# Optimization experiments

Measured on AMD Instinct MI355X. Metric: run time of the kernel, lower is better.

Reference implementation:

```python
import jax, jax.numpy as jnp
import numpy as np

NUM_CLASSES = 2
THRESH = 0.5        # overlap_thresh
NEGPOS = 3          # neg:pos ratio
VAR = (0.1, 0.2)    # cfg['variance']
B, P, O = 64, 32768, 50


def point_form(p):
    # center-size [cx,cy,w,h] -> corner [xmin,ymin,xmax,ymax]
    return jnp.concatenate([p[:, :2] - p[:, 2:] * 0.5, p[:, :2] + p[:, 2:] * 0.5], axis=1)


def iou(a, b):
    # a [O,4], b [P,4] corner form -> [O,P]
    lt = jnp.maximum(a[:, None, :2], b[None, :, :2])
    rb = jnp.minimum(a[:, None, 2:], b[None, :, 2:])
    wh = jnp.clip(rb - lt, 0.0, None)
    inter = wh[..., 0] * wh[..., 1]
    area_a = ((a[:, 2] - a[:, 0]) * (a[:, 3] - a[:, 1]))[:, None]
    area_b = ((b[:, 2] - b[:, 0]) * (b[:, 3] - b[:, 1]))[None, :]
    return inter / (area_a + area_b - inter)


def encode(matched, priors_cs):
    g_cxcy = ((matched[:, :2] + matched[:, 2:]) * 0.5 - priors_cs[:, :2]) / (VAR[0] * priors_cs[:, 2:])
    g_wh = jnp.log((matched[:, 2:] - matched[:, :2]) / priors_cs[:, 2:]) / VAR[1]
    return jnp.concatenate([g_cxcy, g_wh], axis=1)


def match_one(truths, labels, priors_cs, priors_pt):
    ovl = iou(truths, priors_pt)                # [O,P]
    best_prior_idx = jnp.argmax(ovl, axis=1)    # [O] best prior per GT
    best_truth_ovl = jnp.max(ovl, axis=0)       # [P]
    best_truth_idx = jnp.argmax(ovl, axis=0)    # [P]
    best_truth_ovl = best_truth_ovl.at[best_prior_idx].set(2.0)
    best_truth_idx = best_truth_idx.at[best_prior_idx].set(jnp.arange(truths.shape[0]))
    matched = truths[best_truth_idx]            # [P,4]
    conf = jnp.where(best_truth_ovl < THRESH, 0, labels[best_truth_idx])
    return encode(matched, priors_cs), conf


def reference(arm_loc, arm_conf, odm_loc, odm_conf, priors, targets):
    loc_data, conf_data = arm_loc, arm_conf    # use_ARM=False -> ARM branch
    num, num_priors = loc_data.shape[0], loc_data.shape[1]
    truths = targets[..., :4]
    labels = (targets[..., 4] >= 0).astype(jnp.int32)   # num_classes == 2 binarization
    priors_pt = point_form(priors)
    loc_t, conf_t = jax.vmap(lambda t, l: match_one(t, l, priors, priors_pt))(truths, labels)
    loc_t = jax.lax.stop_gradient(loc_t)
    conf_t = jax.lax.stop_gradient(conf_t)
    pos = conf_t > 0                             # [B,P]
    # localization: smooth L1, summed over positives
    d = loc_data - loc_t
    ad = jnp.abs(d)
    sl1 = jnp.where(ad < 1.0, 0.5 * d * d, ad - 0.5)
    loss_l = jnp.sum(sl1 * pos[..., None].astype(loc_data.dtype))
    # per-prior conf loss for hard negative mining
    lse = jax.nn.logsumexp(conf_data, axis=-1)   # [B,P]
    picked = jnp.take_along_axis(conf_data, conf_t[..., None], axis=-1)[..., 0]
    lc = lse - picked                            # NLL per prior
    lc_mine = jnp.where(pos, 0.0, lc)            # zero positives before ranking
    order = jnp.argsort(-lc_mine, axis=1)        # descending sort
    rank = jnp.argsort(order, axis=1)            # rank of each prior
    num_pos = jnp.sum(pos, axis=1, keepdims=True)            # [B,1]
    num_neg = jnp.minimum(NEGPOS * num_pos, num_priors - 1)
    neg = rank < num_neg
    sel = (pos | neg).astype(conf_data.dtype)
    loss_c = jnp.sum(lc * sel)
    N = jnp.sum(num_pos).astype(loc_data.dtype)
    return loss_l / N, loss_c / N


def setup_inputs():
    key = jax.random.key(0)
    ks = jax.random.split(key, 8)
    arm_loc = jax.random.normal(ks[0], (B, P, 4), jnp.float32)
    arm_conf = jax.random.normal(ks[1], (B, P, NUM_CLASSES), jnp.float32)
    odm_loc = jax.random.normal(ks[2], (B, P, 4), jnp.float32)
    odm_conf = jax.random.normal(ks[3], (B, P, NUM_CLASSES), jnp.float32)
    # priors in center-size form
    p_cxcy = jax.random.uniform(ks[4], (P, 2), jnp.float32, 0.05, 0.95)
    p_wh = jax.random.uniform(ks[5], (P, 2), jnp.float32, 0.05, 0.5)
    priors = jnp.concatenate([p_cxcy, p_wh], axis=1)
    # GT boxes in corner form with valid extents, labels >= 0
    t_cxcy = jax.random.uniform(ks[6], (B, O, 2), jnp.float32, 0.2, 0.8)
    t_wh = jax.random.uniform(ks[7], (B, O, 2), jnp.float32, 0.05, 0.3)
    boxes = jnp.concatenate([t_cxcy - t_wh * 0.5, t_cxcy + t_wh * 0.5], axis=-1)
    targets = jnp.concatenate([boxes, jnp.ones((B, O, 1), jnp.float32)], axis=-1)
    return {"arm_loc": arm_loc, "arm_conf": arm_conf, "odm_loc": odm_loc,
            "odm_conf": odm_conf, "priors": priors, "targets": targets}
```

## Files before the change

kernel.cpp:

```cpp
#include <hip/hip_runtime.h>
#include <cstdint>

#pragma clang fp contract(off)

#define BB 64
#define PP 32768
#define OO 50
#define THRESH_F 0.5f
#define VAR0 0.1f
#define VAR1 0.2f
#define NEGPOS_I 3
#define SS 32
#define T1 4
#define NB_P0 256
#define NB_P1 4096
#define NB_P2 2048
#define NCELL 1024
#define PREPB 32

typedef unsigned long long u64;

__device__ __forceinline__ unsigned mpart4(unsigned x) {
    x = (x | (x << 2)) & 0x33u;
    x = (x | (x << 1)) & 0x55u;
    return x;
}
__device__ __forceinline__ int cell_of(float4 pr) {
    int xb = (int)(pr.x * 16.0f); xb = xb < 0 ? 0 : (xb > 15 ? 15 : xb);
    int yb = (int)(pr.y * 16.0f); yb = yb < 0 ? 0 : (yb > 15 ? 15 : yb);
    float s = fmaxf(pr.z, pr.w);
    int wc = s < 0.275f ? 0 : (s < 0.368f ? 1 : (s < 0.44f ? 2 : 3));
    return wc * 256 + (int)(mpart4((unsigned)xb) | (mpart4((unsigned)yb) << 1));
}

__global__ void __launch_bounds__(512)
k_prep(const float4* __restrict__ pri, int* __restrict__ perm, int* __restrict__ iperm,
       float4* __restrict__ zdst, int zn4) {
    __shared__ int cnt[NCELL];
    __shared__ int pref[NCELL];
    __shared__ int scn[512];
    int tid = threadIdx.x, blk = blockIdx.x;
    for (int i = blk * 512 + tid; i < zn4; i += PREPB * 512)
        zdst[i] = make_float4(0.f, 0.f, 0.f, 0.f);
    cnt[tid] = 0; cnt[tid + 512] = 0;
    pref[tid] = 0; pref[tid + 512] = 0;
    __syncthreads();
    int pstart = blk * (PP / PREPB);
    for (int p = tid; p < PP; p += 512) {
        int c = cell_of(pri[p]);
        atomicAdd(&cnt[c], 1);
        if (p < pstart) atomicAdd(&pref[c], 1);
    }
    __syncthreads();
    int a0 = cnt[2 * tid], a1 = cnt[2 * tid + 1];
    int s = a0 + a1;
    scn[tid] = s; __syncthreads();
    for (int off = 1; off < 512; off <<= 1) {
        int v = (tid >= off) ? scn[tid - off] : 0;
        __syncthreads(); scn[tid] += v; __syncthreads();
    }
    int excl = scn[tid] - s;
    cnt[2 * tid]     = excl + pref[2 * tid];
    cnt[2 * tid + 1] = excl + a0 + pref[2 * tid + 1];
    __syncthreads();
    for (int k = 0; k < 2; ++k) {
        int p = pstart + tid * 2 + k;
        int c = cell_of(pri[p]);
        int pos = atomicAdd(&cnt[c], 1);
        perm[pos] = p;
        iperm[p] = pos;
    }
}

#define DPP_MAX(x, ctrl, rmask)                                              \
    {                                                                        \
        int _o = __float_as_int(x);                                          \
        x = fmaxf(x, __int_as_float(__builtin_amdgcn_update_dpp(             \
                _o, _o, (ctrl), (rmask), 0xf, false)));                      \
    }
#define DPP_MINF(x, ctrl, rmask)                                             \
    {                                                                        \
        int _o = __float_as_int(x);                                          \
        x = fminf(x, __int_as_float(__builtin_amdgcn_update_dpp(             \
                _o, _o, (ctrl), (rmask), 0xf, false)));                      \
    }
#define WAVE_MAXF(x) { DPP_MAX(x,0x111,0xf); DPP_MAX(x,0x112,0xf); DPP_MAX(x,0x114,0xf); \
                       DPP_MAX(x,0x118,0xf); DPP_MAX(x,0x142,0xa); DPP_MAX(x,0x143,0xc); }
#define WAVE_MINF(x) { DPP_MINF(x,0x111,0xf); DPP_MINF(x,0x112,0xf); DPP_MINF(x,0x114,0xf); \
                       DPP_MINF(x,0x118,0xf); DPP_MINF(x,0x142,0xa); DPP_MINF(x,0x143,0xc); }

__device__ __forceinline__ float sl1enc(const float* __restrict__ tb,
                                        float4 pr, float4 ld) {
    float gx = ((tb[0] + tb[2]) * 0.5f - pr.x) / (VAR0 * pr.z);
    float gy = ((tb[1] + tb[3]) * 0.5f - pr.y) / (VAR0 * pr.w);
    float gw = logf((tb[2] - tb[0]) / pr.z) / VAR1;
    float gh = logf((tb[3] - tb[1]) / pr.w) / VAR1;
    float g[4] = {gx, gy, gw, gh};
    float l[4] = {ld.x, ld.y, ld.z, ld.w};
    float s = 0.f;
    for (int q = 0; q < 4; ++q) {
        float d = l[q] - g[q];
        float ad = fabsf(d);
        s += (ad < 1.0f) ? 0.5f * d * d : ad - 0.5f;
    }
    return s;
}

__global__ void __launch_bounds__(256, 8)
k_ml(const float* __restrict__ priors, const int* __restrict__ perm,
     const float* __restrict__ targets,
     const float* __restrict__ arm_loc, const float* __restrict__ arm_conf,
     float* __restrict__ lcmP, unsigned char* __restrict__ bpiP,
     u64* __restrict__ bpm,
     float* __restrict__ pll, float* __restrict__ pplc, int* __restrict__ pnp,
     int* __restrict__ Hc0, float* __restrict__ Hs0) {
    __shared__ float4 trP[OO];
    __shared__ float2 trQ[OO];
    __shared__ int   hc[4 * NB_P0];
    __shared__ float hs[4 * NB_P0];
    __shared__ float s1[256]; __shared__ float s2[256]; __shared__ int s3[256];
    int b = (blockIdx.x % 8) * 8 + (blockIdx.y % 8);
    int s = (blockIdx.x / 8) + 4 * (blockIdx.y / 8);
    int tid = threadIdx.x;
    if (tid < OO) {
        const float* tb = &targets[(size_t)(b * OO + tid) * 5];
        float x0 = tb[0], y0 = tb[1], x1 = tb[2], y1 = tb[3];
        trP[tid] = make_float4(x0, y0, x1, y1);
        trQ[tid] = make_float2((x1 - x0) * (y1 - y0), tb[4]);
    }
    for (int i = tid; i < 4 * NB_P0; i += 256) { hc[i] = 0; hs[i] = 0.f; }
    __syncthreads();

    int p0 = s * (256 * T1) + tid * T1;
    int4 o4 = ((const int4*)perm)[p0 >> 2];
    int o_[T1] = {o4.x, o4.y, o4.z, o4.w};
    int omin = min(min(o_[0], o_[1]), min(o_[2], o_[3]));
    float bx0[T1], by0[T1], bx1[T1], by1[T1], aB[T1];
#pragma unroll
    for (int j = 0; j < T1; ++j) {
        float4 pr = ((const float4*)priors)[o_[j]];
        bx0[j] = pr.x - pr.z * 0.5f; by0[j] = pr.y - pr.w * 0.5f;
        bx1[j] = pr.x + pr.z * 0.5f; by1[j] = pr.y + pr.w * 0.5f;
        aB[j] = (bx1[j] - bx0[j]) * (by1[j] - by0[j]);
    }
    float lx0 = fminf(fminf(bx0[0], bx0[1]), fminf(bx0[2], bx0[3]));
    float ly0 = fminf(fminf(by0[0], by0[1]), fminf(by0[2], by0[3]));
    float lx1 = fmaxf(fmaxf(bx1[0], bx1[1]), fmaxf(bx1[2], bx1[3]));
    float ly1 = fmaxf(fmaxf(by1[0], by1[1]), fmaxf(by1[2], by1[3]));
    WAVE_MINF(lx0); WAVE_MINF(ly0); WAVE_MAXF(lx1); WAVE_MAXF(ly1);
    float wx0 = __int_as_float(__builtin_amdgcn_readlane(__float_as_int(lx0), 63));
    float wy0 = __int_as_float(__builtin_amdgcn_readlane(__float_as_int(ly0), 63));
    float wx1 = __int_as_float(__builtin_amdgcn_readlane(__float_as_int(lx1), 63));
    float wy1 = __int_as_float(__builtin_amdgcn_readlane(__float_as_int(ly1), 63));

    float rbv[T1]; int rbi[T1];
#pragma unroll
    for (int j = 0; j < T1; ++j) { rbv[j] = 0.0f; rbi[j] = 0; }

    for (int t = 0; t < OO; ++t) {
        float4 tP = trP[t];
        if (!(tP.z > wx0 && tP.x < wx1 && tP.w > wy0 && tP.y < wy1)) continue;
        float aA = trQ[t].x;
        float I[T1];
#pragma unroll
        for (int j = 0; j < T1; ++j) {
            float ltx = fmaxf(tP.x, bx0[j]), lty = fmaxf(tP.y, by0[j]);
            float rbx = fminf(tP.z, bx1[j]), rby = fminf(tP.w, by1[j]);
            float wx = fmaxf(rbx - ltx, 0.f), wy = fmaxf(rby - lty, 0.f);
            I[j] = wx * wy;
        }
        bool anyl = (I[0] > 0.f) | (I[1] > 0.f) | (I[2] > 0.f) | (I[3] > 0.f);
        if (__any(anyl)) {
            float cbv = 0.0f; int cbo = omin;
#pragma unroll
            for (int j = 0; j < T1; ++j) {
                float v = I[j] / (aA + aB[j] - I[j]);
                if (v > rbv[j]) { rbv[j] = v; rbi[j] = t; }
                if (v > cbv || (v == cbv && o_[j] < cbo)) { cbv = v; cbo = o_[j]; }
            }
            float x = cbv;
            WAVE_MAXF(x);
            float mvf = __int_as_float(__builtin_amdgcn_readlane(__float_as_int(x), 63));
            if (mvf > 0.0f) {
                u64 msk = __ballot(cbv == mvf);
                int ln = (int)__ffsll((long long)msk) - 1;
                int morig = __builtin_amdgcn_readlane(cbo, ln);
                u64 rest = msk & (msk - 1);
                while (rest) {
                    int l2 = (int)__ffsll((long long)rest) - 1;
                    int o2 = __builtin_amdgcn_readlane(cbo, l2);
                    morig = min(morig, o2);
                    rest &= rest - 1;
                }
                if ((tid & 63) == 0) {
                    u64 pk = ((u64)__float_as_uint(mvf) << 32) | (unsigned)(PP - morig);
                    atomicMax(&bpm[b * OO + t], pk);
                }
            }
        }
    }

    size_t bbase = (size_t)b * PP;
    int hb = (tid >> 6) * NB_P0;
    float ll = 0.0f, plc = 0.0f; int np = 0;
    float outv[4]; unsigned pbyte = 0;
#pragma unroll
    for (int c = 0; c < T1; ++c) {
        int o = o_[c]; size_t bo = bbase + o;
        int ti = rbi[c]; float ov = rbv[c];
        float2 cf = ((const float2*)arm_conf)[bo];
        float c0 = cf.x, c1 = cf.y;
        float m = fmaxf(c0, c1);
        float lse = logf(expf(c0 - m) + expf(c1 - m)) + m;
        bool pos = (ov >= THRESH_F) && (trQ[ti].y >= 0.0f);
        float lc = lse - (pos ? c1 : c0);
        outv[c] = pos ? 0.0f : lc;
        pbyte |= (unsigned)((pos ? 0x80u : 0u) | (unsigned)ti) << (8 * c);
        unsigned u = __float_as_uint(outv[c]);
        atomicAdd(&hc[hb + (u >> 23)], 1);
        atomicAdd(&hs[hb + (u >> 23)], outv[c]);
        if (pos) {
            np++; plc += lc;
            float4 pr = ((const float4*)priors)[o];
            float4 ld = ((const float4*)arm_loc)[bo];
            const float4 tv = trP[ti];
            float tb4[4] = {tv.x, tv.y, tv.z, tv.w};
            ll += sl1enc(tb4, pr, ld);
        }
    }
    size_t bq = bbase + p0;
    ((float4*)lcmP)[bq >> 2] = make_float4(outv[0], outv[1], outv[2], outv[3]);
    ((unsigned*)bpiP)[bq >> 2] = pbyte;

    __syncthreads();
    {
        int cv = hc[tid] + hc[NB_P0 + tid] + hc[2*NB_P0 + tid] + hc[3*NB_P0 + tid];
        if (cv) {
            float sv = hs[tid] + hs[NB_P0 + tid] + hs[2*NB_P0 + tid] + hs[3*NB_P0 + tid];
            atomicAdd(&Hc0[b * NB_P0 + tid], cv);
            atomicAdd(&Hs0[b * NB_P0 + tid], sv);
        }
    }
    s1[tid] = ll; s2[tid] = plc; s3[tid] = np;
    __syncthreads();
    for (int st = 128; st > 0; st >>= 1) {
        if (tid < st) { s1[tid] += s1[tid+st]; s2[tid] += s2[tid+st]; s3[tid] += s3[tid+st]; }
        __syncthreads();
    }
    if (tid == 0) {
        pll[s * BB + b] = s1[0];
        pplc[s * BB + b] = s2[0];
        pnp[s * BB + b] = s3[0];
    }
}

__global__ void k_fix(const u64* __restrict__ bpm, const float* __restrict__ targets,
                      const float* __restrict__ arm_loc, const float* __restrict__ arm_conf,
                      const float* __restrict__ priors, const int* __restrict__ iperm,
                      const unsigned char* __restrict__ bpiP, float* __restrict__ lcmP,
                      const float* __restrict__ pll, const float* __restrict__ pplc,
                      const int* __restrict__ pnp,
                      float* __restrict__ llb, float* __restrict__ plcb,
                      int* __restrict__ npb,
                      int* __restrict__ Hc0, float* __restrict__ Hs0) {
    int b = blockIdx.x, j = threadIdx.x;
    int p = -1;
    if (j < OO) {
        unsigned lo = (unsigned)(bpm[b * OO + j] & 0xFFFFFFFFull);
        p = lo ? (PP - (int)lo) : 0;
    }
    bool w = (j < OO);
    for (int jj = 1; jj < OO; ++jj) {
        int pj = __shfl(p, jj, 64);
        if (jj > j && pj == p) w = false;
    }
    float dll = 0.f, dplc = 0.f; int dnp = 0;
    if (w) {
        int pos_ = iperm[p];
        size_t bq = (size_t)b * PP + pos_;
        size_t bo = (size_t)b * PP + p;
        unsigned char ob = bpiP[bq];
        bool old_pos = (ob & 0x80u) != 0;
        int old_ti = ob & 63;
        float2 cf = ((const float2*)arm_conf)[bo];
        float c0 = cf.x, c1 = cf.y;
        float m = fmaxf(c0, c1);
        float lse = logf(expf(c0 - m) + expf(c1 - m)) + m;
        const float* tbj = &targets[(size_t)(b * OO + j) * 5];
        bool new_pos = (tbj[4] >= 0.0f);
        float old_lcm = lcmP[bq];
        float new_lcm = new_pos ? 0.0f : (lse - c0);
        unsigned uo = __float_as_uint(old_lcm), un = __float_as_uint(new_lcm);
        if (uo != un) {
            atomicAdd(&Hc0[b * NB_P0 + (uo >> 23)], -1);
            atomicAdd(&Hs0[b * NB_P0 + (uo >> 23)], -old_lcm);
            atomicAdd(&Hc0[b * NB_P0 + (un >> 23)], 1);
            atomicAdd(&Hs0[b * NB_P0 + (un >> 23)], new_lcm);
            lcmP[bq] = new_lcm;
        }
        float4 pr = ((const float4*)priors)[p];
        float4 ld = ((const float4*)arm_loc)[bo];
        if (old_pos) {
            dnp -= 1; dplc -= (lse - c1);
            dll -= sl1enc(&targets[(size_t)(b * OO + old_ti) * 5], pr, ld);
        }
        if (new_pos) {
            dnp += 1; dplc += (lse - c1);
            dll += sl1enc(tbj, pr, ld);
        }
    }
    float myll = (j < SS) ? pll[j * BB + b] : 0.f;
    float mypl = (j < SS) ? pplc[j * BB + b] : 0.f;
    int   mynp = (j < SS) ? pnp[j * BB + b] : 0;
    dll += myll; dplc += mypl; dnp += mynp;
    for (int st = 32; st >= 1; st >>= 1) {
        dll += __shfl_down(dll, st, 64);
        dplc += __shfl_down(dplc, st, 64);
        dnp += __shfl_down(dnp, st, 64);
    }
    if (j == 0) {
        llb[b] = dll;
        plcb[b] = dplc;
        npb[b] = dnp;
    }
}

__global__ void __launch_bounds__(256)
k_sel(const float* __restrict__ lcmP,
      const float* __restrict__ llb, const float* __restrict__ plcb,
      const int* __restrict__ npb,
      const int* __restrict__ Hc0, const float* __restrict__ Hs0,
      float* __restrict__ gacc, int* __restrict__ gcnt,
      float* __restrict__ out) {
    __shared__ int hc[NB_P1]; __shared__ float hs[NB_P1];
    __shared__ int sc[256]; __shared__ float sf[256];
    __shared__ int s_chunk, s_r; __shared__ float s_S; __shared__ unsigned s_pref;
    int b = blockIdx.x, tid = threadIdx.x;
    const float4* v4 = (const float4*)(lcmP + (size_t)b * PP);

    {
        int c = Hc0[b * NB_P0 + tid];
        float f = Hs0[b * NB_P0 + tid];
        sc[tid] = c; sf[tid] = f;
        if (tid == 0) {
            int k = NEGPOS_I * npb[b]; if (k > PP - 1) k = PP - 1;
            s_r = k; s_S = 0.f;
        }
        __syncthreads();
        for (int off = 1; off < 256; off <<= 1) {
            int cv = (tid + off < 256) ? sc[tid + off] : 0;
            float fv = (tid + off < 256) ? sf[tid + off] : 0.f;
            __syncthreads(); sc[tid] += cv; sf[tid] += fv; __syncthreads();
        }
        int r = s_r;
        int nxt = (tid == 255) ? 0 : sc[tid + 1];
        if (sc[tid] >= r && nxt < r) s_chunk = tid;
        __syncthreads();
        if (tid == 0) {
            int ch = s_chunk;
            s_pref = (unsigned)ch;
            s_r = r - ((ch == 255) ? 0 : sc[ch + 1]);
            s_S = (ch == 255) ? 0.f : sf[ch + 1];
        }
        __syncthreads();
    }
    {
        for (int i = tid; i < NB_P1; i += 256) { hc[i] = 0; hs[i] = 0.f; }
        __syncthreads();
        unsigned pref = s_pref;
        for (int it = 0; it < 32; ++it) {
            float4 x = v4[it * 256 + tid];
            float xs[4] = {x.x, x.y, x.z, x.w};
            for (int c2 = 0; c2 < 4; ++c2) {
                unsigned u = __float_as_uint(xs[c2]);
                if ((u >> 23) == pref) {
                    atomicAdd(&hc[(u >> 11) & 4095u], 1);
                    atomicAdd(&hs[(u >> 11) & 4095u], xs[c2]);
                }
            }
        }
        __syncthreads();
        int c = 0; float f = 0.f; int base = tid * 16;
        for (int i = 0; i < 16; ++i) { c += hc[base + i]; f += hs[base + i]; }
        sc[tid] = c; sf[tid] = f; __syncthreads();
        for (int off = 1; off < 256; off <<= 1) {
            int cv = (tid + off < 256) ? sc[tid + off] : 0;
            float fv = (tid + off < 256) ? sf[tid + off] : 0.f;
            __syncthreads(); sc[tid] += cv; sf[tid] += fv; __syncthreads();
        }
        int r = s_r;
        int nxt = (tid == 255) ? 0 : sc[tid + 1];
        if (sc[tid] >= r && nxt < r) s_chunk = tid;
        __syncthreads();
        if (tid == 0) {
            int ch = s_chunk;
            int r2 = r - ((ch == 255) ? 0 : sc[ch + 1]);
            float S2 = s_S + ((ch == 255) ? 0.f : sf[ch + 1]);
            int binSel = ch * 16;
            for (int i = 15; i >= 0; --i) {
                int bin = ch * 16 + i; int cbn = hc[bin];
                if (r2 <= cbn) { binSel = bin; break; }
                r2 -= cbn; S2 += hs[bin];
            }
            s_pref = (s_pref << 12) | (unsigned)binSel; s_r = r2; s_S = S2;
        }
        __syncthreads();
    }
    {
        for (int i = tid; i < NB_P2; i += 256) { hc[i] = 0; hs[i] = 0.f; }
        __syncthreads();
        unsigned pref = s_pref;
        for (int it = 0; it < 32; ++it) {
            float4 x = v4[it * 256 + tid];
            float xs[4] = {x.x, x.y, x.z, x.w};
            for (int c2 = 0; c2 < 4; ++c2) {
                unsigned u = __float_as_uint(xs[c2]);
                if ((u >> 11) == pref) {
                    atomicAdd(&hc[u & 2047u], 1);
                    atomicAdd(&hs[u & 2047u], xs[c2]);
                }
            }
        }
        __syncthreads();
        int c = 0; float f = 0.f; int base = tid * 8;
        for (int i = 0; i < 8; ++i) { c += hc[base + i]; f += hs[base + i]; }
        sc[tid] = c; sf[tid] = f; __syncthreads();
        for (int off = 1; off < 256; off <<= 1) {
            int cv = (tid + off < 256) ? sc[tid + off] : 0;
            float fv = (tid + off < 256) ? sf[tid + off] : 0.f;
            __syncthreads(); sc[tid] += cv; sf[tid] += fv; __syncthreads();
        }
        int r = s_r;
        int nxt = (tid == 255) ? 0 : sc[tid + 1];
        if (sc[tid] >= r && nxt < r) s_chunk = tid;
        __syncthreads();
        if (tid == 0) {
            int ch = s_chunk;
            int r2 = r - ((ch == 255) ? 0 : sc[ch + 1]);
            float S2 = s_S + ((ch == 255) ? 0.f : sf[ch + 1]);
            int binSel = ch * 8;
            for (int i = 7; i >= 0; --i) {
                int bin = ch * 8 + i; int cbn = hc[bin];
                if (r2 <= cbn) { binSel = bin; break; }
                r2 -= cbn; S2 += hs[bin];
            }
            unsigned tb = (s_pref << 11) | (unsigned)binSel;
            float tval = __uint_as_float(tb);
            float ccb = plcb[b] + S2 + (float)r2 * tval;
            float llv = llb[b]; int npv = npb[b];
            atomicAdd(&gacc[0], llv);
            atomicAdd(&gacc[1], ccb);
            atomicAdd(&gcnt[0], npv);
            __threadfence();
            int tk = atomicAdd(&gcnt[1], 1);
            if (tk == BB - 1) {
                __threadfence();
                float llt = atomicAdd(&gacc[0], 0.f);
                float cct = atomicAdd(&gacc[1], 0.f);
                int npt = atomicAdd(&gcnt[0], 0);
                float N = (float)npt;
                out[0] = llt / N;
                out[1] = cct / N;
            }
        }
    }
}

extern "C" void kernel_launch(void* const* d_in, const int* in_sizes, int n_in,
                              void* d_out, int out_size, void* d_ws, size_t ws_size,
                              hipStream_t stream) {
    const float* arm_loc  = (const float*)d_in[0];
    const float* arm_conf = (const float*)d_in[1];
    const float* priors   = (const float*)d_in[4];
    const float* targets  = (const float*)d_in[5];
    float* out = (float*)d_out;

    char* w = (char*)d_ws;
    float* lcmP = (float*)w;  w += sizeof(float) * (size_t)BB * PP;
    unsigned char* bpiP = (unsigned char*)w; w += (size_t)BB * PP;
    char* zbase = w;
    int*   Hc0 = (int*)w;    w += sizeof(int)   * BB * NB_P0;
    float* Hs0 = (float*)w;  w += sizeof(float) * BB * NB_P0;
    u64*   bpm = (u64*)w;    w += sizeof(u64)   * BB * OO;
    float* gacc = (float*)w; w += sizeof(float) * 2;
    int*   gcnt = (int*)w;   w += sizeof(int)   * 2;
    size_t zbytes = (size_t)(w - zbase);
    int*   perm  = (int*)w;  w += sizeof(int) * PP;
    int*   iperm = (int*)w;  w += sizeof(int) * PP;
    float* pll  = (float*)w; w += sizeof(float) * BB * SS;
    float* pplc = (float*)w; w += sizeof(float) * BB * SS;
    int*   pnp  = (int*)w;   w += sizeof(int)   * BB * SS;
    float* llb  = (float*)w; w += sizeof(float) * BB;
    float* plcb = (float*)w; w += sizeof(float) * BB;
    int*   npb  = (int*)w;   w += sizeof(int)   * BB;

    int zn4 = (int)(zbytes / 16);
    k_prep<<<PREPB, 512, 0, stream>>>((const float4*)priors, perm, iperm,
                                      (float4*)zbase, zn4);
    k_ml<<<dim3(SS, BB), 256, 0, stream>>>(priors, perm, targets, arm_loc, arm_conf,
                                           lcmP, bpiP, bpm, pll, pplc, pnp, Hc0, Hs0);
    k_fix<<<BB, 64, 0, stream>>>(bpm, targets, arm_loc, arm_conf, priors, iperm,
                                 bpiP, lcmP, pll, pplc, pnp, llb, plcb, npb, Hc0, Hs0);
    k_sel<<<BB, 256, 0, stream>>>(lcmP, llb, plcb, npb, Hc0, Hs0, gacc, gcnt, out);
}
```

Measured before the change: 271.9 us.

## Split prior binning into histogram and scatter kernels, ballot-skip targets, batch loads

Replaces the single prep kernel, in which every block scanned all priors, with two kernels: one builds a cell histogram per block, the other prefix-sums those histograms and scatters priors using global atomic cursors. The match kernel now builds a wave ballot mask of targets that overlap the wave's bounding box and iterates only over its set bits, instead of testing every target in the loop. The radix-select histogram passes load four float4 values per iteration to raise memory-level parallelism. One side effect is that the order of priors within a cell now depends on atomic timing, so the permutation is nondeterministic, and an extra kernel launch is added.

```diff
diff --git a/kernel.cpp b/kernel.cpp
--- a/kernel.cpp
+++ b/kernel.cpp
@@ -16,7 +16,6 @@
 #define NB_P1 4096
 #define NB_P2 2048
 #define NCELL 1024
-#define PREPB 32
 
 typedef unsigned long long u64;
 
@@ -33,42 +32,52 @@
     return wc * 256 + (int)(mpart4((unsigned)xb) | (mpart4((unsigned)yb) << 1));
 }
 
-__global__ void __launch_bounds__(512)
-k_prep(const float4* __restrict__ pri, int* __restrict__ perm, int* __restrict__ iperm,
-       float4* __restrict__ zdst, int zn4) {
-    __shared__ int cnt[NCELL];
-    __shared__ int pref[NCELL];
-    __shared__ int scn[512];
+__global__ void __launch_bounds__(256)
+k_phist(const float4* __restrict__ pri, int* __restrict__ cnt32,
+        int* __restrict__ cursor) {
+    __shared__ int lc[NCELL];
     int tid = threadIdx.x, blk = blockIdx.x;
-    for (int i = blk * 512 + tid; i < zn4; i += PREPB * 512)
+    for (int i = tid; i < NCELL; i += 256) lc[i] = 0;
+    if (blk == 0)
+        for (int i = tid; i < NCELL; i += 256) cursor[i] = 0;
+    __syncthreads();
+    int p = blk * 1024 + tid * 4;
+    for (int j = 0; j < 4; ++j)
+        atomicAdd(&lc[cell_of(pri[p + j])], 1);
+    __syncthreads();
+    for (int i = tid; i < NCELL; i += 256) cnt32[blk * NCELL + i] = lc[i];
+}
+
+__global__ void __launch_bounds__(256)
+k_pss(const float4* __restrict__ pri, const int* __restrict__ cnt32,
+      int* __restrict__ cursor, int* __restrict__ perm, int* __restrict__ iperm,
+      float4* __restrict__ zdst, int zn4) {
+    __shared__ int sc[256];
+    __shared__ int sbase[NCELL];
+    int tid = threadIdx.x;
+    for (int i = blockIdx.x * 256 + tid; i < zn4; i += 32 * 256)
         zdst[i] = make_float4(0.f, 0.f, 0.f, 0.f);
-    cnt[tid] = 0; cnt[tid + 512] = 0;
-    pref[tid] = 0; pref[tid + 512] = 0;
+    int a[4]; int s = 0;
+    for (int i = 0; i < 4; ++i) {
+        int c = tid * 4 + i;
+        int v = 0;
+        for (int r = 0; r < 32; ++r) v += cnt32[r * NCELL + c];
+        a[i] = v; s += v;
+    }
+    sc[tid] = s; __syncthreads();
+    for (int off = 1; off < 256; off <<= 1) {
+        int v = (tid >= off) ? sc[tid - off] : 0;
+        __syncthreads(); sc[tid] += v; __syncthreads();
+    }
+    int excl = sc[tid] - s;
+    for (int i = 0; i < 4; ++i) { sbase[tid * 4 + i] = excl; excl += a[i]; }
     __syncthreads();
-    int pstart = blk * (PP / PREPB);
-    for (int p = tid; p < PP; p += 512) {
-        int c = cell_of(pri[p]);
-        atomicAdd(&cnt[c], 1);
-        if (p < pstart) atomicAdd(&pref[c], 1);
-    }
-    __syncthreads();
-    int a0 = cnt[2 * tid], a1 = cnt[2 * tid + 1];
-    int s = a0 + a1;
-    scn[tid] = s; __syncthreads();
-    for (int off = 1; off < 512; off <<= 1) {
-        int v = (tid >= off) ? scn[tid - off] : 0;
-        __syncthreads(); scn[tid] += v; __syncthreads();
-    }
-    int excl = scn[tid] - s;
-    cnt[2 * tid]     = excl + pref[2 * tid];
-    cnt[2 * tid + 1] = excl + a0 + pref[2 * tid + 1];
-    __syncthreads();
-    for (int k = 0; k < 2; ++k) {
-        int p = pstart + tid * 2 + k;
-        int c = cell_of(pri[p]);
-        int pos = atomicAdd(&cnt[c], 1);
-        perm[pos] = p;
-        iperm[p] = pos;
+    int p = blockIdx.x * 1024 + tid * 4;
+    for (int j = 0; j < 4; ++j) {
+        int c = cell_of(pri[p + j]);
+        int pos = sbase[c] + atomicAdd(&cursor[c], 1);
+        perm[pos] = p + j;
+        iperm[p + j] = pos;
     }
 }
 
@@ -153,13 +162,24 @@
     float wx1 = __int_as_float(__builtin_amdgcn_readlane(__float_as_int(lx1), 63));
     float wy1 = __int_as_float(__builtin_amdgcn_readlane(__float_as_int(ly1), 63));
 
+    u64 smask;
+    {
+        int lane = tid & 63;
+        bool sv = false;
+        if (lane < OO) {
+            float4 tt = trP[lane];
+            sv = (tt.z > wx0 && tt.x < wx1 && tt.w > wy0 && tt.y < wy1);
+        }
+        smask = __ballot(sv);
+    }
+
     float rbv[T1]; int rbi[T1];
 #pragma unroll
     for (int j = 0; j < T1; ++j) { rbv[j] = 0.0f; rbi[j] = 0; }
 
-    for (int t = 0; t < OO; ++t) {
+    for (u64 mm = smask; mm; mm &= mm - 1) {
+        int t = (int)__ffsll((long long)mm) - 1;
         float4 tP = trP[t];
-        if (!(tP.z > wx0 && tP.x < wx1 && tP.w > wy0 && tP.y < wy1)) continue;
         float aA = trQ[t].x;
         float I[T1];
 #pragma unroll
@@ -368,14 +388,19 @@
         for (int i = tid; i < NB_P1; i += 256) { hc[i] = 0; hs[i] = 0.f; }
         __syncthreads();
         unsigned pref = s_pref;
-        for (int it = 0; it < 32; ++it) {
-            float4 x = v4[it * 256 + tid];
-            float xs[4] = {x.x, x.y, x.z, x.w};
-            for (int c2 = 0; c2 < 4; ++c2) {
-                unsigned u = __float_as_uint(xs[c2]);
-                if ((u >> 23) == pref) {
-                    atomicAdd(&hc[(u >> 11) & 4095u], 1);
-                    atomicAdd(&hs[(u >> 11) & 4095u], xs[c2]);
+        for (int it = 0; it < 8; ++it) {
+            float4 xs4[4];
+#pragma unroll
+            for (int q = 0; q < 4; ++q) xs4[q] = v4[it * 1024 + q * 256 + tid];
+#pragma unroll
+            for (int q = 0; q < 4; ++q) {
+                float xs[4] = {xs4[q].x, xs4[q].y, xs4[q].z, xs4[q].w};
+                for (int c2 = 0; c2 < 4; ++c2) {
+                    unsigned u = __float_as_uint(xs[c2]);
+                    if ((u >> 23) == pref) {
+                        atomicAdd(&hc[(u >> 11) & 4095u], 1);
+                        atomicAdd(&hs[(u >> 11) & 4095u], xs[c2]);
+                    }
                 }
             }
         }
@@ -410,14 +435,19 @@
         for (int i = tid; i < NB_P2; i += 256) { hc[i] = 0; hs[i] = 0.f; }
         __syncthreads();
         unsigned pref = s_pref;
-        for (int it = 0; it < 32; ++it) {
-            float4 x = v4[it * 256 + tid];
-            float xs[4] = {x.x, x.y, x.z, x.w};
-            for (int c2 = 0; c2 < 4; ++c2) {
-                unsigned u = __float_as_uint(xs[c2]);
-                if ((u >> 11) == pref) {
-                    atomicAdd(&hc[u & 2047u], 1);
-                    atomicAdd(&hs[u & 2047u], xs[c2]);
+        for (int it = 0; it < 8; ++it) {
+            float4 xs4[4];
+#pragma unroll
+            for (int q = 0; q < 4; ++q) xs4[q] = v4[it * 1024 + q * 256 + tid];
+#pragma unroll
+            for (int q = 0; q < 4; ++q) {
+                float xs[4] = {xs4[q].x, xs4[q].y, xs4[q].z, xs4[q].w};
+                for (int c2 = 0; c2 < 4; ++c2) {
+                    unsigned u = __float_as_uint(xs[c2]);
+                    if ((u >> 11) == pref) {
+                        atomicAdd(&hc[u & 2047u], 1);
+                        atomicAdd(&hs[u & 2047u], xs[c2]);
+                    }
                 }
             }
         }
@@ -485,6 +515,8 @@
     float* gacc = (float*)w; w += sizeof(float) * 2;
     int*   gcnt = (int*)w;   w += sizeof(int)   * 2;
     size_t zbytes = (size_t)(w - zbase);
+    int*   cnt32 = (int*)w;  w += sizeof(int) * 32 * NCELL;
+    int*   cursor = (int*)w; w += sizeof(int) * NCELL;
     int*   perm  = (int*)w;  w += sizeof(int) * PP;
     int*   iperm = (int*)w;  w += sizeof(int) * PP;
     float* pll  = (float*)w; w += sizeof(float) * BB * SS;
@@ -495,8 +527,9 @@
     int*   npb  = (int*)w;   w += sizeof(int)   * BB;
 
     int zn4 = (int)(zbytes / 16);
-    k_prep<<<PREPB, 512, 0, stream>>>((const float4*)priors, perm, iperm,
-                                      (float4*)zbase, zn4);
+    k_phist<<<PP / 1024, 256, 0, stream>>>((const float4*)priors, cnt32, cursor);
+    k_pss<<<PP / 1024, 256, 0, stream>>>((const float4*)priors, cnt32, cursor,
+                                         perm, iperm, (float4*)zbase, zn4);
     k_ml<<<dim3(SS, BB), 256, 0, stream>>>(priors, perm, targets, arm_loc, arm_conf,
                                            lcmP, bpiP, bpm, pll, pplc, pnp, Hc0, Hs0);
     k_fix<<<BB, 64, 0, stream>>>(bpm, targets, arm_loc, arm_conf, priors, iperm,
```

New measurement: 248.9 us. 1.09x faster.
